# Performance work log

Hardware: AMD Instinct MI355X
Metric: run time of the kernel (lower is better)

Reference implementation:

```python
import jax, jax.numpy as jnp
import numpy as np

# ---- straight-through binary quantizers (custom VJP matches torch autograd.Functions) ----
@jax.custom_vjp
def bq(x):
    return jnp.sign(x)
def _bq_fwd(x):
    return jnp.sign(x), x
def _bq_bwd(x, g):
    return (g * ((x > -1.0) & (x < 1.0)).astype(g.dtype),)
bq.defvjp(_bq_fwd, _bq_bwd)

@jax.custom_vjp
def bq_quad(x):
    return jnp.sign(x)
def _bqq_fwd(x):
    return jnp.sign(x), x
def _bqq_bwd(x, g):
    return (jnp.maximum(2.0 - jnp.abs(2.0 * x), 0.0) * g,)
bq_quad.defvjp(_bqq_fwd, _bqq_bwd)

def bilinear(x, W, s, b):
    # BiLinear: row-centered sign weights scaled by learned per-row factor, sign activations
    Wc = W - jnp.mean(W, axis=-1, keepdims=True)
    Wb = s * bq(Wc)                      # (out, in)
    return bq(x) @ Wb.T + b

def selective_scan(u, delta, A, Bs, Cs, D, delta_bias):
    # u, delta: (B,K,Dn,L); A: (K,Dn,N); Bs,Cs: (B,K,N,L); D, delta_bias: (K,Dn)
    Bn, K, Dn, L = u.shape
    N = A.shape[-1]
    delta = jax.nn.softplus(delta + delta_bias[None, :, :, None])
    def step(h, inp):
        ut, dt, Bt, Ct = inp             # (B,K,Dn),(B,K,Dn),(B,K,N),(B,K,N)
        dA = jnp.exp(dt[..., None] * A[None])
        h = dA * h + (dt * ut)[..., None] * Bt[:, :, None, :]
        y = jnp.einsum('bkdn,bkn->bkd', h, Ct)
        return h, y
    h0 = jnp.zeros((Bn, K, Dn, N), u.dtype)
    _, ys = jax.lax.scan(step, h0,
                         (u.transpose(3, 0, 1, 2), delta.transpose(3, 0, 1, 2),
                          Bs.transpose(3, 0, 1, 2), Cs.transpose(3, 0, 1, 2)))
    y = ys.transpose(1, 2, 3, 0)         # (B,K,Dn,L)
    return y + D[None, :, :, None] * u

def _forward(x, W_in, b_in, s_in, move0_b, conv_W, conv_b, rp_b0, prelu_a, rp_b1,
             Wl, bl, sl, Wd, bd, sd, dt_bias, A_logs, Ds, ln_w, ln_b, W_out, b_out, s_out):
    Bn, H, Wi, dm = x.shape
    Dn = conv_W.shape[0]
    K = 4
    N = A_logs.shape[1]
    R = Wd.shape[2]
    L = H * Wi
    xz = bilinear(x, W_in, s_in, b_in)                  # (B,H,W,2*Dn)
    xp, z = jnp.split(xz, 2, axis=-1)
    xc = xp.transpose(0, 3, 1, 2)                       # (B,Dn,H,W)
    # BConv2d: move0 bias -> sign (quad STE) -> binary conv -> RPReLU -> residual
    t = bq_quad(xc + move0_b[None, :, None, None])
    sc = jax.lax.stop_gradient(jnp.mean(jnp.abs(conv_W), axis=(1, 2, 3), keepdims=True))
    cw = jnp.clip(conv_W, -1.0, 1.0)
    Wb = jax.lax.stop_gradient(sc * jnp.sign(conv_W) - cw) + cw
    t = jax.lax.conv_general_dilated(t, Wb, (1, 1), [(1, 1), (1, 1)],
                                     dimension_numbers=('NCHW', 'OIHW', 'NCHW'))
    t = t + conv_b[None, :, None, None]
    t = t + rp_b0[None, :, None, None]
    t = jnp.where(t >= 0, t, prelu_a[None, :, None, None] * t)
    t = t + rp_b1[None, :, None, None] + xc
    xconv = jax.nn.silu(t)
    # 4-direction scan inputs
    x_flat = xconv.reshape(Bn, Dn, L)
    x_tr = xconv.transpose(0, 1, 3, 2).reshape(Bn, Dn, L)
    x_hwwh = jnp.stack([x_flat, x_tr], axis=1)
    xs = jnp.concatenate([x_hwwh, jnp.flip(x_hwwh, axis=-1)], axis=1)   # (B,K,Dn,L)
    # NOTE: torch does .view(B,L,-1) on contiguous (B,Dn,L) slices = raw reshape (not transpose)
    xin = xs.reshape(Bn, K, L, Dn)
    x_dbl = jax.vmap(bilinear, in_axes=(1, 0, 0, 0), out_axes=1)(xin, Wl, sl, bl)  # (B,K,L,R+2N)
    x_dbl = x_dbl.transpose(0, 1, 3, 2)                                 # (B,K,R+2N,L)
    dts_r, Bs, Cs = jnp.split(x_dbl, [R, R + N], axis=2)
    dts_in = dts_r.reshape(Bn, K, L, R)  # raw reshape, matches torch .view
    dts = jax.vmap(bilinear, in_axes=(1, 0, 0, 0), out_axes=1)(dts_in, Wd, sd, bd)  # (B,K,L,Dn)
    dts = dts.transpose(0, 1, 3, 2)                                     # (B,K,Dn,L)
    A = -jnp.exp(A_logs).reshape(K, Dn, N)
    out_y = selective_scan(xs, dts, A, Bs, Cs, Ds.reshape(K, Dn), dt_bias.reshape(K, Dn))
    inv_y = jnp.flip(out_y[:, 2:4], axis=-1)
    wh_y = out_y[:, 1].reshape(Bn, Dn, Wi, H).transpose(0, 1, 3, 2).reshape(Bn, Dn, L)
    invwh_y = inv_y[:, 1].reshape(Bn, Dn, Wi, H).transpose(0, 1, 3, 2).reshape(Bn, Dn, L)
    y = out_y[:, 0] + inv_y[:, 0] + wh_y + invwh_y                      # (B,Dn,L)
    y = y.transpose(0, 2, 1).reshape(Bn, H, Wi, Dn)
    mu = jnp.mean(y, axis=-1, keepdims=True)
    var = jnp.var(y, axis=-1, keepdims=True)
    y = (y - mu) / jnp.sqrt(var + 1e-5) * ln_w + ln_b                   # LayerNorm eps=1e-5
    y = y * jax.nn.silu(z)
    return bilinear(y, W_out, s_out, b_out)

def setup_inputs():
    key = jax.random.key(0)
    ks = jax.random.split(key, 12)
    B, H, Wi, dm = 4, 64, 64, 96
    Dn, N, R, K = 192, 16, 6, 4
    u = lambda k, sh, a: jax.random.uniform(k, sh, jnp.float32, -a, a)
    x = jax.random.normal(ks[0], (B, H, Wi, dm), jnp.float32)
    W_in = u(ks[1], (2 * Dn, dm), 0.015)
    b_in = u(ks[2], (2 * Dn,), 0.01)
    s_in = jnp.mean(jnp.abs(W_in), axis=1, keepdims=True)
    move0_b = jnp.zeros((Dn,), jnp.float32)
    conv_W = 0.05 * jax.random.normal(ks[3], (Dn, Dn, 3, 3), jnp.float32)
    conv_b = u(ks[4], (Dn,), 0.01)
    rp_b0 = jnp.zeros((Dn,), jnp.float32)
    prelu_a = 0.25 * jnp.ones((Dn,), jnp.float32)
    rp_b1 = jnp.zeros((Dn,), jnp.float32)
    Wl = u(ks[5], (K, R + 2 * N, Dn), 0.015)
    bl = u(ks[6], (K, R + 2 * N), 0.01)
    sl = jnp.mean(jnp.abs(Wl), axis=2, keepdims=True)
    std = R ** -0.5
    Wd = u(ks[7], (K, Dn, R), std)
    bd = u(ks[8], (K, Dn), 0.01)
    sd = jnp.mean(jnp.abs(Wd), axis=2, keepdims=True)
    dt = jnp.exp(jax.random.uniform(ks[9], (K * Dn,), jnp.float32)
                 * (np.log(0.1) - np.log(0.001)) + np.log(0.001))
    dt = jnp.clip(dt, 1e-4, None)
    dt_bias = dt + jnp.log(-jnp.expm1(-dt))
    A_logs = jnp.tile(jnp.log(jnp.arange(1, N + 1, dtype=jnp.float32))[None, :], (K * Dn, 1))
    Ds = jnp.ones((K * Dn,), jnp.float32)
    ln_w = jnp.ones((Dn,), jnp.float32)
    ln_b = jnp.zeros((Dn,), jnp.float32)
    W_out = u(ks[10], (dm, Dn), 0.015)
    b_out = u(ks[11], (dm,), 0.01)
    s_out = jnp.mean(jnp.abs(W_out), axis=1, keepdims=True)
    return dict(x=x, W_in=W_in, b_in=b_in, s_in=s_in, move0_b=move0_b, conv_W=conv_W,
                conv_b=conv_b, rp_b0=rp_b0, prelu_a=prelu_a, rp_b1=rp_b1, Wl=Wl, bl=bl,
                sl=sl, Wd=Wd, bd=bd, sd=sd, dt_bias=dt_bias, A_logs=A_logs, Ds=Ds,
                ln_w=ln_w, ln_b=ln_b, W_out=W_out, b_out=b_out, s_out=s_out)

def reference(x, W_in, b_in, s_in, move0_b, conv_W, conv_b, rp_b0, prelu_a, rp_b1,
              Wl, bl, sl, Wd, bd, sd, dt_bias, A_logs, Ds, ln_w, ln_b, W_out, b_out, s_out):
    return _forward(x, W_in, b_in, s_in, move0_b, conv_W, conv_b, rp_b0, prelu_a, rp_b1,
                    Wl, bl, sl, Wd, bd, sd, dt_bias, A_logs, Ds, ln_w, ln_b, W_out, b_out, s_out)
```

## Files before the change

### kernel.cpp

```cpp
#include <hip/hip_runtime.h>
#include <math.h>
#include <stdint.h>

#define BB 4
#define HH 64
#define WW2 64
#define DM 96
#define DN 192
#define KK 4
#define NN 16
#define RR 6
#define LL 4096
#define RN 38

#define LOG2E 1.4426950408889634f
#define LN2   0.6931471805599453f

#define OFF_WDB      0
#define OFF_WCS      4608
#define OFF_WAUX     15360
#define OFF_WSC      16896
#define OFF_WBIB     17088
#define OFF_WOUTB    18240
#define OFF_WLBB     18816
#define OFF_XBP      19728
#define OFF_PXS      19728
#define OFF_PXIN     412944
#define OFF_XP       462096
#define OFF_XCONV    3607824
#define OFF_XCT      6753552
#define OFF_HEND     462096
#define OFF_YA       9899280
#define OFF_SSUM     22482192
#define OFF_GE       22875408
#define OFF_GSG      23268624

#define PLANE 4356
#define NCH 128
#define CHUNK 32

__device__ __forceinline__ float softplusf(float v) {
  return fmaxf(v, 0.f) + LN2 * log2f(1.f + exp2f(-fabsf(v) * LOG2E));
}
__device__ __forceinline__ float siluf(float v) {
  return v / (1.f + expf(-v));
}
__device__ __forceinline__ float waveAllSum(float s) {
  #pragma unroll
  for (int off = 32; off; off >>= 1) s += __shfl_xor(s, off, 64);
  return s;
}

__global__ __launch_bounds__(64) void k_prep(
    const float* __restrict__ W_in, const float* __restrict__ s_in,
    const float* __restrict__ W_out, const float* __restrict__ s_out,
    const float* __restrict__ Wl, const float* __restrict__ sl,
    const float* __restrict__ Wd, const float* __restrict__ sd,
    const float* __restrict__ convW, float* __restrict__ ws) {
  __shared__ float srow[1728];
  int r = blockIdx.x, lane = threadIdx.x;
  if (r < 384) {
    const float* row = W_in + r * DM;
    float s = 0.f;
    for (int c = lane; c < DM; c += 64) s += row[c];
    s = waveAllSum(s);
    float mean = s / (float)DM;
    if (lane < 3) {
      uint32_t wv = 0;
      #pragma unroll
      for (int i = 0; i < 32; ++i) wv |= (row[lane * 32 + i] - mean > 0.f ? 1u : 0u) << i;
      ((uint32_t*)(ws + OFF_WBIB))[r * 3 + lane] = wv;
    }
  } else if (r < 480) {
    int m = r - 384;
    const float* row = W_out + m * DN;
    float s = 0.f;
    for (int c = lane; c < DN; c += 64) s += row[c];
    s = waveAllSum(s);
    float mean = s / (float)DN;
    if (lane < 6) {
      uint32_t wv = 0;
      #pragma unroll
      for (int i = 0; i < 32; ++i) wv |= (row[lane * 32 + i] - mean > 0.f ? 1u : 0u) << i;
      ((uint32_t*)(ws + OFF_WOUTB))[m * 6 + lane] = wv;
    }
  } else if (r < 632) {
    int idx = r - 480;
    const float* row = Wl + idx * DN;
    float s = 0.f;
    for (int c = lane; c < DN; c += 64) s += row[c];
    s = waveAllSum(s);
    float mean = s / (float)DN;
    if (lane < 6) {
      uint32_t wv = 0;
      #pragma unroll
      for (int i = 0; i < 32; ++i) wv |= (row[lane * 32 + i] - mean > 0.f ? 1u : 0u) << i;
      ((uint32_t*)(ws + OFF_WLBB))[idx * 6 + lane] = wv;
    }
  } else if (r < 1400) {
    int idx = r - 632;
    const float* row = Wd + idx * RR;
    float s = (lane < RR) ? row[lane] : 0.f;
    s = waveAllSum(s);
    float mean = s / (float)RR;
    unsigned long long mb = __ballot((lane < RR) && (row[lane] - mean > 0.f));
    if (lane == 0) {
      ((uint32_t*)(ws + OFF_WDB))[idx] = (uint32_t)mb & 0x3Fu;
      (ws + OFF_WDB)[768 + idx] = sd[idx];
    }
  } else if (r < 1592) {
    int o = r - 1400;
    const float* row = convW + o * 1728;
    float s = 0.f;
    for (int j = lane; j < 1728; j += 64) {
      float v = row[j];
      srow[j] = v;
      s += fabsf(v);
    }
    s = waveAllSum(s);
    __syncthreads();
    float sc = s / 1728.f;
    uint32_t* wb = (uint32_t*)(ws + OFF_WCS);
    int* aux = (int*)(ws + OFF_WAUX);
    float* scf = ws + OFF_WSC;
    uint32_t word = 0;
    if (lane < 54) {
      int cw = lane / 9, tap = lane % 9;
      #pragma unroll
      for (int i = 0; i < 32; ++i)
        word |= (srow[(cw * 32 + i) * 9 + tap] > 0.f ? 1u : 0u) << i;
      wb[o * 56 + lane] = word;
    } else if (lane < 56) {
      wb[o * 56 + lane] = 0u;
    }
    int pc = (lane < 54) ? 2 * (int)__popc(word) - 32 : 0;
    int tapid = lane % 9;
    int wst = 0;
    #pragma unroll
    for (int cw = 0; cw < 6; ++cw) wst += __shfl(pc, cw * 9 + tapid, 64);
    int w_t[9];
    #pragma unroll
    for (int t9 = 0; t9 < 9; ++t9) w_t[t9] = __shfl(wst, t9, 64);
    if (lane == 0) {
      aux[o * 8 + 0] = w_t[0] + w_t[3] + w_t[6];
      aux[o * 8 + 1] = w_t[2] + w_t[5] + w_t[8];
      aux[o * 8 + 2] = w_t[0] + w_t[1] + w_t[2];
      aux[o * 8 + 3] = w_t[6] + w_t[7] + w_t[8];
      aux[o * 8 + 4] = w_t[0];
      aux[o * 8 + 5] = w_t[2];
      aux[o * 8 + 6] = w_t[6];
      aux[o * 8 + 7] = w_t[8];
      scf[o] = sc;
    }
  } else {
    int p = r - 1592;
    uint32_t* plane = (uint32_t*)(ws + OFF_XBP) + (size_t)p * PLANE;
    for (int i = lane; i < 66; i += 64) {
      plane[i] = 0u;
      plane[65 * 66 + i] = 0u;
    }
    for (int i = lane; i < 64; i += 64) {
      plane[(i + 1) * 66] = 0u;
      plane[(i + 1) * 66 + 65] = 0u;
    }
  }
}

__global__ __launch_bounds__(384) void k_bilin_in(
    const float* __restrict__ x, const float* __restrict__ b_in,
    const float* __restrict__ s_in, const float* __restrict__ move0,
    const float* __restrict__ ws, float* __restrict__ xp,
    uint32_t* __restrict__ pxin, uint32_t* __restrict__ xb) {
  __shared__ uint32_t spx[16 * 3];
  __shared__ float sxz[192 * 17];
  __shared__ float smv[DN];
  int p0 = blockIdx.x * 16;
  if (threadIdx.x < 48) {
    int pix = threadIdx.x / 3, wd = threadIdx.x % 3;
    const float* base = x + (size_t)(p0 + pix) * DM + wd * 32;
    uint32_t wv = 0;
    #pragma unroll
    for (int i = 0; i < 32; ++i) wv |= (base[i] > 0.f ? 1u : 0u) << i;
    spx[pix * 3 + wd] = wv;
  }
  if (threadIdx.x < DN) smv[threadIdx.x] = move0[threadIdx.x];
  __syncthreads();
  int half = threadIdx.x / 192;
  int o = threadIdx.x - half * 192;
  uint32_t w0, w1, w2;
  {
    const uint32_t* wb = (const uint32_t*)(ws + OFF_WBIB) + o * 3;
    w0 = wb[0]; w1 = wb[1]; w2 = wb[2];
  }
  float bias = b_in[o], sc = s_in[o];
  #pragma unroll
  for (int pp = 0; pp < 8; ++pp) {
    int pix = half * 8 + pp;
    int P = (int)__popc(spx[pix * 3 + 0] ^ w0) + (int)__popc(spx[pix * 3 + 1] ^ w1) +
            (int)__popc(spx[pix * 3 + 2] ^ w2);
    sxz[o * 17 + pix] = bias + sc * (float)(DM - 2 * P);
  }
  __syncthreads();
  int b = p0 >> 12, l0 = p0 & 4095;
  for (int f = threadIdx.x; f < DN * 16; f += 384) {
    int od = f >> 4, pix = f & 15;
    xp[((size_t)(b * DN + od)) * LL + l0 + pix] = sxz[od * 17 + pix];
  }
  if (threadIdx.x < 48) {
    int pix = threadIdx.x / 3, wd = threadIdx.x % 3;
    pxin[(size_t)(p0 + pix) * 3 + wd] = spx[pix * 3 + wd];
  }
  if (threadIdx.x < 96) {
    int pix = threadIdx.x / 6, cw = threadIdx.x % 6;
    uint32_t wv = 0;
    #pragma unroll
    for (int i = 0; i < 32; ++i) {
      int dch = cw * 32 + i;
      wv |= ((sxz[dch * 17 + pix] + smv[dch] > 0.f) ? 1u : 0u) << i;
    }
    int l = l0 + pix, h = l >> 6, w = l & 63;
    uint32_t* plane = xb + (size_t)(b * 6 + cw) * PLANE;
    plane[(h + 1) * 66 + 1 + w] = wv;
  }
}

__global__ __launch_bounds__(256) void k_conv(
    const uint32_t* __restrict__ xb, const float* __restrict__ xc,
    const uint32_t* __restrict__ wbits, const int* __restrict__ aux,
    const float* __restrict__ scf, const float* __restrict__ conv_b,
    const float* __restrict__ rp_b0, const float* __restrict__ prelu_a,
    const float* __restrict__ rp_b1, float* __restrict__ xconv) {
  int ocg = blockIdx.x & 3;
  int og = (blockIdx.x >> 2) & 3;
  int stripe = (blockIdx.x >> 4) & 15;
  int b = blockIdx.x >> 8;
  int w = threadIdx.x & 63, r = threadIdx.x >> 6;
  int h = stripe * 4 + r;
  int obase = og * 48 + ocg * 12;

  __shared__ uint32_t swb[12 * 56];
  __shared__ int saux[12 * 8];
  __shared__ float sconst[12 * 4];
  for (int i = threadIdx.x; i < 12 * 56; i += 256) swb[i] = wbits[obase * 56 + i];
  for (int i = threadIdx.x; i < 12 * 8; i += 256) saux[i] = aux[obase * 8 + i];
  if (threadIdx.x < 12) {
    int o = obase + threadIdx.x;
    sconst[threadIdx.x * 4 + 0] = scf[o];
    sconst[threadIdx.x * 4 + 1] = conv_b[o] + rp_b0[o];
    sconst[threadIdx.x * 4 + 2] = prelu_a[o];
    sconst[threadIdx.x * 4 + 3] = rp_b1[o];
  }

  uint32_t xw[6][9];
  const uint32_t* xpb = xb + (size_t)b * 6 * PLANE;
  #pragma unroll
  for (int cw = 0; cw < 6; ++cw) {
    const uint32_t* plane = xpb + cw * PLANE + (h + 1) * 66 + (w + 1);
    #pragma unroll
    for (int dy = 0; dy < 3; ++dy) {
      #pragma unroll
      for (int dx = 0; dx < 3; ++dx)
        xw[cw][dy * 3 + dx] = plane[(dy - 1) * 66 + (dx - 1)];
    }
  }
  bool isL = (w == 0), isR = (w == 63);
  bool isT = (h == 0), isB = (h == 63);
  const float* xcp = xc + ((size_t)(b * DN + obase)) * LL + h * 64 + w;
  float* xop = xconv + ((size_t)(b * DN + obase)) * LL + h * 64 + w;
  __syncthreads();

  #pragma unroll 1
  for (int oc = 0; oc < 12; ++oc) {
    const uint32_t* wp = &swb[oc * 56];
    int P = 0;
    #pragma unroll
    for (int cw = 0; cw < 6; ++cw) {
      int pp = 0;
      #pragma unroll
      for (int t = 0; t < 9; ++t) pp += (int)__popc(wp[cw * 9 + t] ^ xw[cw][t]);
      P += pp;
    }
    int corr = isL ? saux[oc * 8 + 0] : (isR ? saux[oc * 8 + 1] : 0);
    if (isT) {
      corr += saux[oc * 8 + 2];
      if (isL) corr -= saux[oc * 8 + 4];
      if (isR) corr -= saux[oc * 8 + 5];
    }
    if (isB) {
      corr += saux[oc * 8 + 3];
      if (isL) corr -= saux[oc * 8 + 6];
      if (isR) corr -= saux[oc * 8 + 7];
    }
    float acc = sconst[oc * 4 + 0] * (float)(1728 - 2 * P + corr);
    float t = acc + sconst[oc * 4 + 1];
    t = (t >= 0.f) ? t : sconst[oc * 4 + 2] * t;
    t += sconst[oc * 4 + 3] + *xcp;
    *xop = siluf(t);
    xcp += LL; xop += LL;
  }
}

__global__ __launch_bounds__(256) void k_bits_xpose(const float* __restrict__ xconv,
                                                    uint32_t* __restrict__ pxs,
                                                    float* __restrict__ xct) {
  __shared__ float tile[64][65];
  if (blockIdx.x < 768) {
    int bd = blockIdx.x;
    int b = bd / DN, dch = bd - b * DN;
    const float* img = xconv + (size_t)bd * LL;
    for (int i = threadIdx.x; i < LL; i += 256)
      tile[i >> 6][i & 63] = img[i];
    __syncthreads();
    int lane = threadIdx.x & 63;
    #pragma unroll
    for (int k = 0; k < 4; ++k) {
      size_t wbase = ((size_t)((b * KK + k) * DN + dch)) * 128;
      for (int j = threadIdx.x; j < LL; j += 256) {
        float v;
        if (k == 0)      v = tile[j >> 6][j & 63];
        else if (k == 1) v = tile[j & 63][j >> 6];
        else if (k == 2) { int t2 = 4095 - j; v = tile[t2 >> 6][t2 & 63]; }
        else             { int t2 = 4095 - j; v = tile[t2 & 63][t2 >> 6]; }
        unsigned long long m = __ballot(v > 0.f);
        if (lane == 0)       pxs[wbase + (j >> 5)] = (uint32_t)m;
        else if (lane == 32) pxs[wbase + (j >> 5)] = (uint32_t)(m >> 32);
      }
    }
  } else {
    int idx = blockIdx.x - 768;
    int ts = idx & 63;
    int rest = idx >> 6;
    int dg = rest % 3;
    int b = rest / 3;
    int d0 = dg * 64, t0 = ts * 64;
    for (int i = threadIdx.x; i < 4096; i += 256) {
      int dd = i >> 6, tt = i & 63;
      tile[dd][tt] = xconv[((size_t)(b * DN + d0 + dd)) * LL + t0 + tt];
    }
    __syncthreads();
    for (int i = threadIdx.x; i < 4096; i += 256) {
      int tt = i >> 6, dd = i & 63;
      xct[((size_t)(b * LL + t0 + tt)) * DN + d0 + dd] = tile[dd][tt];
    }
  }
}

__device__ __forceinline__ void rpowers(float r, float* a) {
  float r2 = r * r, r3 = r2 * r, r4 = r2 * r2, r8 = r4 * r4;
  a[0] = r;       a[1] = r2;      a[2] = r3;      a[3] = r4;
  a[4] = r4 * r;  a[5] = r4 * r2; a[6] = r4 * r3; a[7] = r8;
  a[8] = r8 * r;  a[9] = r8 * r2; a[10] = r8 * r3; a[11] = r8 * r4;
  a[12] = r8 * a[4]; a[13] = r8 * a[5]; a[14] = r8 * a[6]; a[15] = r8 * r8;
}

__device__ __forceinline__ int rowstep(int k) {
  return (k == 0) ? DN : (k == 1) ? 64 * DN : (k == 2) ? -DN : -64 * DN;
}
__device__ __forceinline__ int rowbase(int k, int tb) {
  int r0 = (k >= 2) ? (4095 - tb) : tb;
  if (k & 1) r0 = ((r0 & 63) << 6) | (r0 >> 6);
  return r0 * DN;
}

__global__ __launch_bounds__(192) void k_scan_a(
    const float* __restrict__ xct, const uint32_t* __restrict__ pxs,
    const float* __restrict__ ws, const float* __restrict__ bl,
    const float* __restrict__ sl, const float* __restrict__ bd,
    const float* __restrict__ dt_bias, const float* __restrict__ A_logs,
    float* __restrict__ hend, float* __restrict__ Ssum) {
  int c = blockIdx.x & (NCH - 1);
  int bk = blockIdx.x >> 7;
  int k = bk & 3, b = bk >> 2;
  int d = threadIdx.x;
  int t0 = c << 5;
  __shared__ uint32_t sdtm[CHUNK];
  __shared__ uint32_t spxr[CHUNK * 6];
  __shared__ uint32_t swl[RN * 6];
  __shared__ float sblv[RN], sslv[RN];
  __shared__ float4 sB4[CHUNK * 4];
  __shared__ float sDV[7 * 192], sR[7 * 192];
  float* sBf = (float*)sB4;
  const uint32_t* ppx = pxs + (size_t)bk * 24576;
  spxr[d] = ppx[t0 * 6 + d];
  for (int i = d; i < RN * 6; i += 192) swl[i] = ((const uint32_t*)(ws + OFF_WLBB))[k * RN * 6 + i];
  if (d < RN) {
    sblv[d] = bl[k * RN + d];
    sslv[d] = sl[k * RN + d];
  }
  __syncthreads();
  if (d < CHUNK) {
    uint32_t m = 0;
    int fbase = (t0 + d) * 6;
    #pragma unroll
    for (int r = 0; r < 6; ++r) {
      int f = fbase + r;
      int o = f >> 12, l = f & 4095;
      const uint32_t* prow = ppx + l * 6;
      int P = 0;
      #pragma unroll
      for (int j = 0; j < 6; ++j) P += (int)__popc(prow[j] ^ swl[o * 6 + j]);
      float val = sblv[o] + sslv[o] * (float)(DN - 2 * P);
      m |= (val > 0.f ? 1u : 0u) << r;
    }
    sdtm[d] = m;
  }
  for (int i = d; i < CHUNK * 16; i += 192) {
    int t = i >> 4, n = i & 15;
    int o = RR + n;
    int P = 0;
    #pragma unroll
    for (int j = 0; j < 6; ++j) P += (int)__popc(spxr[t * 6 + j] ^ swl[o * 6 + j]);
    sBf[t * 16 + n] = sblv[o] + sslv[o] * (float)(DN - 2 * P);
  }
  uint32_t w6 = ((const uint32_t*)(ws + OFF_WDB))[k * DN + d];
  float sdvv = (ws + OFF_WDB)[768 + k * DN + d];
  float biasd = bd[k * DN + d] + dt_bias[k * DN + d];
  #pragma unroll
  for (int pc = 0; pc < 7; ++pc) {
    float dv = softplusf(biasd + sdvv * (float)(RR - 2 * pc));
    sDV[pc * 192 + d] = dv;
    sR[pc * 192 + d] = exp2f(-dv * LOG2E);
  }
  float Araw[16];
  bool fok = true;
  {
    const float* ap = A_logs + (k * DN + d) * NN;
    #pragma unroll
    for (int n = 0; n < NN; ++n) {
      Araw[n] = -expf(ap[n]);
      fok = fok && (fabsf(Araw[n] + (float)(n + 1)) < 1e-3f);
    }
  }
  bool fastpath = (__ballot(fok) == ~0ull);
  float An[16];
  if (!fastpath) {
    #pragma unroll
    for (int n = 0; n < NN; ++n) An[n] = Araw[n] * LOG2E;
  }
  float h[16];
  #pragma unroll
  for (int n = 0; n < NN; ++n) h[n] = 0.f;
  float S = 0.f;
  int ubase = b * (LL * DN) + d;
  int rstep = rowstep(k);
  __syncthreads();
  #pragma unroll 1
  for (int seg = 0; seg < 4; ++seg) {
    int rbase = rowbase(k, t0 + seg * 8);
    float uu[8];
    #pragma unroll
    for (int i = 0; i < 8; ++i) uu[i] = xct[ubase + rbase + i * rstep];
    #pragma unroll
    for (int i = 0; i < 8; ++i) {
      int t = seg * 8 + i;
      float uv = uu[i];
      int pc = (int)__popc(sdtm[t] ^ w6);
      float dv = sDV[pc * 192 + d];
      S += dv;
      float du = dv * uv;
      if (fastpath) {
        float rv = sR[pc * 192 + d];
        float a[16];
        rpowers(rv, a);
        #pragma unroll
        for (int g = 0; g < 4; ++g) {
          float4 bv = sB4[t * 4 + g];
          h[4 * g + 0] = a[4 * g + 0] * h[4 * g + 0] + du * bv.x;
          h[4 * g + 1] = a[4 * g + 1] * h[4 * g + 1] + du * bv.y;
          h[4 * g + 2] = a[4 * g + 2] * h[4 * g + 2] + du * bv.z;
          h[4 * g + 3] = a[4 * g + 3] * h[4 * g + 3] + du * bv.w;
        }
      } else {
        #pragma unroll
        for (int g = 0; g < 4; ++g) {
          float4 bv = sB4[t * 4 + g];
          float a0 = exp2f(dv * An[4 * g + 0]);
          float a1 = exp2f(dv * An[4 * g + 1]);
          float a2 = exp2f(dv * An[4 * g + 2]);
          float a3 = exp2f(dv * An[4 * g + 3]);
          h[4 * g + 0] = a0 * h[4 * g + 0] + du * bv.x;
          h[4 * g + 1] = a1 * h[4 * g + 1] + du * bv.y;
          h[4 * g + 2] = a2 * h[4 * g + 2] + du * bv.z;
          h[4 * g + 3] = a3 * h[4 * g + 3] + du * bv.w;
        }
      }
    }
  }
  float* hp = hend + (size_t)c * 49152 + (size_t)(bk * DN + d) * 16;
  #pragma unroll
  for (int n = 0; n < NN; n += 4)
    *(float4*)(hp + n) = make_float4(h[n], h[n + 1], h[n + 2], h[n + 3]);
  Ssum[c * 3072 + bk * DN + d] = S;
}

__global__ __launch_bounds__(256) void k_scan_b1(
    const float* __restrict__ A_logs, const float* __restrict__ Ssum,
    float* __restrict__ hend, float* __restrict__ gE, float* __restrict__ gSG) {
  int g = blockIdx.x / 192;
  int blk = blockIdx.x - g * 192;
  int tid = blk * 256 + threadIdx.x;
  int bkd = tid >> 4, n = tid & 15;
  int bk = bkd / DN, d = bkd - bk * DN;
  int k = bk & 3;
  float An2 = -expf(A_logs[(k * DN + d) * NN + n]) * LOG2E;
  int c0 = g * 16;
  float E = 0.f, SG = 0.f;
  float Sc = Ssum[c0 * 3072 + bkd];
  float he = hend[(size_t)c0 * 49152 + tid];
  #pragma unroll 1
  for (int j = 0; j < 16; ++j) {
    int c = c0 + j;
    float Sn = 0.f, hn = 0.f;
    if (j < 15) {
      Sn = Ssum[(c + 1) * 3072 + bkd];
      hn = hend[(size_t)(c + 1) * 49152 + tid];
    }
    hend[(size_t)c * 49152 + tid] = E;
    E = exp2f(An2 * Sc) * E + he;
    SG += Sc;
    Sc = Sn; he = hn;
  }
  gE[(size_t)g * 49152 + tid] = E;
  if (n == 0) gSG[g * 3072 + bkd] = SG;
}

__global__ __launch_bounds__(256) void k_scan_b2(
    const float* __restrict__ A_logs, const float* __restrict__ Ssum,
    float* __restrict__ hend, const float* __restrict__ gE,
    const float* __restrict__ gSG) {
  int g = blockIdx.x / 192;
  if (g == 0) return;
  int blk = blockIdx.x - g * 192;
  int tid = blk * 256 + threadIdx.x;
  int bkd = tid >> 4, n = tid & 15;
  int bk = bkd / DN, d = bkd - bk * DN;
  int k = bk & 3;
  float An2 = -expf(A_logs[(k * DN + d) * NN + n]) * LOG2E;
  float H = 0.f;
  #pragma unroll 1
  for (int j = 0; j < g; ++j) {
    float Aj = exp2f(An2 * gSG[j * 3072 + bkd]);
    H = Aj * H + gE[(size_t)j * 49152 + tid];
  }
  int c0 = g * 16;
  float Spre = 0.f;
  #pragma unroll 1
  for (int j = 0; j < 16; ++j) {
    int c = c0 + j;
    hend[(size_t)c * 49152 + tid] += exp2f(An2 * Spre) * H;
    Spre += Ssum[c * 3072 + bkd];
  }
}

__global__ __launch_bounds__(192) void k_scan_c(
    const float* __restrict__ xct, const uint32_t* __restrict__ pxs,
    const float* __restrict__ ws, const float* __restrict__ bl,
    const float* __restrict__ sl, const float* __restrict__ bd,
    const float* __restrict__ dt_bias, const float* __restrict__ A_logs,
    const float* __restrict__ Ds, float* __restrict__ yA,
    const float* __restrict__ h0buf) {
  int c = blockIdx.x & (NCH - 1);
  int bk = blockIdx.x >> 7;
  int k = bk & 3, b = bk >> 2;
  int d = threadIdx.x;
  int t0 = c << 5;
  __shared__ uint32_t sdtm[CHUNK];
  __shared__ uint32_t spxr[CHUNK * 6];
  __shared__ uint32_t swl[RN * 6];
  __shared__ float sblv[RN], sslv[RN];
  __shared__ float4 sB4[CHUNK * 4];
  __shared__ float4 sC4[CHUNK * 4];
  __shared__ float sDV[7 * 192], sR[7 * 192];
  float* sBf = (float*)sB4;
  float* sCf = (float*)sC4;
  const uint32_t* ppx = pxs + (size_t)bk * 24576;
  spxr[d] = ppx[t0 * 6 + d];
  for (int i = d; i < RN * 6; i += 192) swl[i] = ((const uint32_t*)(ws + OFF_WLBB))[k * RN * 6 + i];
  if (d < RN) {
    sblv[d] = bl[k * RN + d];
    sslv[d] = sl[k * RN + d];
  }
  __syncthreads();
  if (d < CHUNK) {
    uint32_t m = 0;
    int fbase = (t0 + d) * 6;
    #pragma unroll
    for (int r = 0; r < 6; ++r) {
      int f = fbase + r;
      int o = f >> 12, l = f & 4095;
      const uint32_t* prow = ppx + l * 6;
      int P = 0;
      #pragma unroll
      for (int j = 0; j < 6; ++j) P += (int)__popc(prow[j] ^ swl[o * 6 + j]);
      float val = sblv[o] + sslv[o] * (float)(DN - 2 * P);
      m |= (val > 0.f ? 1u : 0u) << r;
    }
    sdtm[d] = m;
  }
  for (int i = d; i < CHUNK * 32; i += 192) {
    int t = i >> 5, nn = i & 31;
    int o = RR + nn;
    int P = 0;
    #pragma unroll
    for (int j = 0; j < 6; ++j) P += (int)__popc(spxr[t * 6 + j] ^ swl[o * 6 + j]);
    float val = sblv[o] + sslv[o] * (float)(DN - 2 * P);
    if (nn < 16) sBf[t * 16 + nn] = val;
    else         sCf[t * 16 + (nn - 16)] = val;
  }
  uint32_t w6 = ((const uint32_t*)(ws + OFF_WDB))[k * DN + d];
  float sdvv = (ws + OFF_WDB)[768 + k * DN + d];
  float biasd = bd[k * DN + d] + dt_bias[k * DN + d];
  float Dd = Ds[k * DN + d];
  #pragma unroll
  for (int pc = 0; pc < 7; ++pc) {
    float dv = softplusf(biasd + sdvv * (float)(RR - 2 * pc));
    sDV[pc * 192 + d] = dv;
    sR[pc * 192 + d] = exp2f(-dv * LOG2E);
  }
  float Araw[16];
  bool fok = true;
  {
    const float* ap = A_logs + (k * DN + d) * NN;
    #pragma unroll
    for (int n = 0; n < NN; ++n) {
      Araw[n] = -expf(ap[n]);
      fok = fok && (fabsf(Araw[n] + (float)(n + 1)) < 1e-3f);
    }
  }
  bool fastpath = (__ballot(fok) == ~0ull);
  float An[16];
  if (!fastpath) {
    #pragma unroll
    for (int n = 0; n < NN; ++n) An[n] = Araw[n] * LOG2E;
  }
  float h[16];
  {
    const float* hp = h0buf + (size_t)c * 49152 + (size_t)(bk * DN + d) * 16;
    #pragma unroll
    for (int n = 0; n < NN; n += 4) {
      float4 v = *(const float4*)(hp + n);
      h[n] = v.x; h[n + 1] = v.y; h[n + 2] = v.z; h[n + 3] = v.w;
    }
  }
  int ubase = b * (LL * DN) + d;
  int ybase = bk * (LL * DN) + d;
  int rstep = rowstep(k);
  __syncthreads();
  #pragma unroll 1
  for (int seg = 0; seg < 4; ++seg) {
    int rbase = rowbase(k, t0 + seg * 8);
    float uu[8];
    #pragma unroll
    for (int i = 0; i < 8; ++i) uu[i] = xct[ubase + rbase + i * rstep];
    #pragma unroll
    for (int i = 0; i < 8; ++i) {
      int t = seg * 8 + i;
      float uv = uu[i];
      int pc = (int)__popc(sdtm[t] ^ w6);
      float dv = sDV[pc * 192 + d];
      float du = dv * uv;
      float p[4];
      #pragma unroll
      for (int g = 0; g < 4; ++g) p[g] = 0.f;
      if (fastpath) {
        float rv = sR[pc * 192 + d];
        float a[16];
        rpowers(rv, a);
        #pragma unroll
        for (int g = 0; g < 4; ++g) {
          float4 bv = sB4[t * 4 + g];
          float4 cv = sC4[t * 4 + g];
          h[4 * g + 0] = a[4 * g + 0] * h[4 * g + 0] + du * bv.x;
          h[4 * g + 1] = a[4 * g + 1] * h[4 * g + 1] + du * bv.y;
          h[4 * g + 2] = a[4 * g + 2] * h[4 * g + 2] + du * bv.z;
          h[4 * g + 3] = a[4 * g + 3] * h[4 * g + 3] + du * bv.w;
          p[g] += cv.x * h[4 * g + 0];
          p[g] += cv.y * h[4 * g + 1];
          p[g] += cv.z * h[4 * g + 2];
          p[g] += cv.w * h[4 * g + 3];
        }
      } else {
        #pragma unroll
        for (int g = 0; g < 4; ++g) {
          float4 bv = sB4[t * 4 + g];
          float4 cv = sC4[t * 4 + g];
          float a0 = exp2f(dv * An[4 * g + 0]);
          float a1 = exp2f(dv * An[4 * g + 1]);
          float a2 = exp2f(dv * An[4 * g + 2]);
          float a3 = exp2f(dv * An[4 * g + 3]);
          h[4 * g + 0] = a0 * h[4 * g + 0] + du * bv.x;
          h[4 * g + 1] = a1 * h[4 * g + 1] + du * bv.y;
          h[4 * g + 2] = a2 * h[4 * g + 2] + du * bv.z;
          h[4 * g + 3] = a3 * h[4 * g + 3] + du * bv.w;
          p[g] += cv.x * h[4 * g + 0];
          p[g] += cv.y * h[4 * g + 1];
          p[g] += cv.z * h[4 * g + 2];
          p[g] += cv.w * h[4 * g + 3];
        }
      }
      float yv = Dd * uv + ((p[0] + p[1]) + (p[2] + p[3]));
      yA[ybase + rbase + i * rstep] = yv;
    }
  }
}

__global__ __launch_bounds__(256) void k_ln_out(
    const float* __restrict__ yA, const uint32_t* __restrict__ pxin,
    const float* __restrict__ b_in, const float* __restrict__ s_in,
    const float* __restrict__ ln_w, const float* __restrict__ ln_b,
    const float* __restrict__ ws, const float* __restrict__ b_out,
    const float* __restrict__ s_out, float* __restrict__ out) {
  __shared__ float ty[16 * 193];
  __shared__ float ps[256];
  __shared__ float smu[16], srs[16];
  __shared__ float slw[DN], slb[DN];
  __shared__ uint32_t ybits[16 * 6];
  __shared__ uint32_t swo[96 * 6];
  __shared__ float sb[96], ssc[96];
  __shared__ uint32_t szw[DN * 3];
  __shared__ float szb[DN], szs[DN];
  __shared__ uint32_t spxt[16 * 3];
  int b = blockIdx.x >> 8;
  int l0 = (blockIdx.x & 255) << 4;
  if (threadIdx.x < DN) {
    slw[threadIdx.x] = ln_w[threadIdx.x];
    slb[threadIdx.x] = ln_b[threadIdx.x];
    szb[threadIdx.x] = b_in[DN + threadIdx.x];
    szs[threadIdx.x] = s_in[DN + threadIdx.x];
  }
  for (int i = threadIdx.x; i < 96 * 6; i += 256) swo[i] = ((const uint32_t*)(ws + OFF_WOUTB))[i];
  for (int i = threadIdx.x; i < DN * 3; i += 256) szw[i] = ((const uint32_t*)(ws + OFF_WBIB))[DN * 3 + i];
  if (threadIdx.x < 96) {
    sb[threadIdx.x] = b_out[threadIdx.x];
    ssc[threadIdx.x] = s_out[threadIdx.x];
  }
  if (threadIdx.x < 48) spxt[threadIdx.x] = pxin[(size_t)(b * LL + l0) * 3 + threadIdx.x];
  const float* y0 = yA + (size_t)(b * 4 + 0) * (LL * DN) + (size_t)l0 * DN;
  const float* y1 = yA + (size_t)(b * 4 + 1) * (LL * DN) + (size_t)l0 * DN;
  const float* y2 = yA + (size_t)(b * 4 + 2) * (LL * DN) + (size_t)l0 * DN;
  const float* y3 = yA + (size_t)(b * 4 + 3) * (LL * DN) + (size_t)l0 * DN;
  for (int i = threadIdx.x; i < 16 * DN; i += 256) {
    int lc = i / DN, dd = i - lc * DN;
    size_t off = (size_t)lc * DN + dd;
    ty[lc * 193 + dd] = y0[off] + y1[off] + y2[off] + y3[off];
  }
  __syncthreads();
  int lc = threadIdx.x & 15, part = threadIdx.x >> 4;
  float s = 0.f;
  for (int d = part * 12; d < part * 12 + 12; ++d) s += ty[lc * 193 + d];
  ps[threadIdx.x] = s;
  __syncthreads();
  if (threadIdx.x < 16) {
    float m = 0.f;
    #pragma unroll
    for (int p = 0; p < 16; ++p) m += ps[p * 16 + threadIdx.x];
    smu[threadIdx.x] = m / (float)DN;
  }
  __syncthreads();
  float mu = smu[lc];
  float q = 0.f;
  for (int d = part * 12; d < part * 12 + 12; ++d) {
    float v = ty[lc * 193 + d] - mu; q += v * v;
  }
  ps[threadIdx.x] = q;
  __syncthreads();
  if (threadIdx.x < 16) {
    float vv = 0.f;
    #pragma unroll
    for (int p = 0; p < 16; ++p) vv += ps[p * 16 + threadIdx.x];
    srs[threadIdx.x] = rsqrtf(vv / (float)DN + 1e-5f);
  }
  __syncthreads();
  if (threadIdx.x < 16 * 6) {
    int lc2 = threadIdx.x / 6, wd = threadIdx.x % 6;
    float mu2 = smu[lc2], rs2 = srs[lc2];
    uint32_t px0 = spxt[lc2 * 3 + 0], px1 = spxt[lc2 * 3 + 1], px2 = spxt[lc2 * 3 + 2];
    uint32_t wv = 0;
    #pragma unroll
    for (int i = 0; i < 32; ++i) {
      int dd = wd * 32 + i;
      float lnv = (ty[lc2 * 193 + dd] - mu2) * rs2 * slw[dd] + slb[dd];
      int P = (int)__popc(px0 ^ szw[dd * 3 + 0]) + (int)__popc(px1 ^ szw[dd * 3 + 1]) +
              (int)__popc(px2 ^ szw[dd * 3 + 2]);
      float zv = szb[dd] + szs[dd] * (float)(DM - 2 * P);
      wv |= ((lnv * zv > 0.f) ? 1u : 0u) << i;
    }
    ybits[lc2 * 6 + wd] = wv;
  }
  __syncthreads();
  float* op = out + (size_t)(b * LL + l0) * DM;
  for (int oi = threadIdx.x; oi < 16 * DM; oi += 256) {
    int pr = oi / DM, m = oi % DM;
    int P = 0;
    #pragma unroll
    for (int j = 0; j < 6; ++j) P += (int)__popc(ybits[pr * 6 + j] ^ swo[m * 6 + j]);
    op[(size_t)pr * DM + m] = sb[m] + ssc[m] * (float)(DN - 2 * P);
  }
}

extern "C" void kernel_launch(void* const* d_in, const int* in_sizes, int n_in,
                              void* d_out, int out_size, void* d_ws, size_t ws_size,
                              hipStream_t stream) {
  const float* x       = (const float*)d_in[0];
  const float* W_in    = (const float*)d_in[1];
  const float* b_in    = (const float*)d_in[2];
  const float* s_in    = (const float*)d_in[3];
  const float* move0_b = (const float*)d_in[4];
  const float* conv_W  = (const float*)d_in[5];
  const float* conv_b  = (const float*)d_in[6];
  const float* rp_b0   = (const float*)d_in[7];
  const float* prelu_a = (const float*)d_in[8];
  const float* rp_b1   = (const float*)d_in[9];
  const float* Wl      = (const float*)d_in[10];
  const float* bl      = (const float*)d_in[11];
  const float* sl      = (const float*)d_in[12];
  const float* Wd      = (const float*)d_in[13];
  const float* bd      = (const float*)d_in[14];
  const float* sd      = (const float*)d_in[15];
  const float* dt_bias = (const float*)d_in[16];
  const float* A_logs  = (const float*)d_in[17];
  const float* Ds      = (const float*)d_in[18];
  const float* ln_w    = (const float*)d_in[19];
  const float* ln_b    = (const float*)d_in[20];
  const float* W_out   = (const float*)d_in[21];
  const float* b_out   = (const float*)d_in[22];
  const float* s_out   = (const float*)d_in[23];
  float* ws  = (float*)d_ws;
  float* out = (float*)d_out;

  hipLaunchKernelGGL(k_prep, dim3(1616), dim3(64), 0, stream,
                     W_in, s_in, W_out, s_out, Wl, sl, Wd, sd, conv_W, ws);
  hipLaunchKernelGGL(k_bilin_in, dim3(1024), dim3(384), 0, stream,
                     x, b_in, s_in, move0_b, ws, ws + OFF_XP,
                     (uint32_t*)(ws + OFF_PXIN), (uint32_t*)(ws + OFF_XBP));
  hipLaunchKernelGGL(k_conv, dim3(1024), dim3(256), 0, stream,
                     (const uint32_t*)(ws + OFF_XBP), ws + OFF_XP,
                     (const uint32_t*)(ws + OFF_WCS), (const int*)(ws + OFF_WAUX),
                     ws + OFF_WSC, conv_b, rp_b0, prelu_a, rp_b1,
                     ws + OFF_XCONV);
  hipLaunchKernelGGL(k_bits_xpose, dim3(1536), dim3(256), 0, stream,
                     ws + OFF_XCONV, (uint32_t*)(ws + OFF_PXS), ws + OFF_XCT);
  hipLaunchKernelGGL(k_scan_a, dim3(2048), dim3(192), 0, stream,
                     ws + OFF_XCT, (const uint32_t*)(ws + OFF_PXS), ws, bl, sl,
                     bd, dt_bias, A_logs, ws + OFF_HEND, ws + OFF_SSUM);
  hipLaunchKernelGGL(k_scan_b1, dim3(1536), dim3(256), 0, stream,
                     A_logs, ws + OFF_SSUM, ws + OFF_HEND, ws + OFF_GE, ws + OFF_GSG);
  hipLaunchKernelGGL(k_scan_b2, dim3(1536), dim3(256), 0, stream,
                     A_logs, ws + OFF_SSUM, ws + OFF_HEND, ws + OFF_GE, ws + OFF_GSG);
  hipLaunchKernelGGL(k_scan_c, dim3(2048), dim3(192), 0, stream,
                     ws + OFF_XCT, (const uint32_t*)(ws + OFF_PXS), ws, bl, sl,
                     bd, dt_bias, A_logs, Ds, ws + OFF_YA, ws + OFF_HEND);
  hipLaunchKernelGGL(k_ln_out, dim3(1024), dim3(256), 0, stream,
                     ws + OFF_YA, (const uint32_t*)(ws + OFF_PXIN), b_in, s_in,
                     ln_w, ln_b, ws, b_out, s_out, out);
}
```

Baseline: 277.3 us.

## Recompute input projection inside conv and use fewer, longer scan chunks

The float input-projection tensor is no longer written by the bilinear kernel and read back by the conv kernel. Instead the conv kernel recomputes each channel's value from the packed sign bits and binarized weights with a popcount. Separately, the chunked selective scan now uses 64 chunks of 64 steps instead of 128 chunks of 32. This halves the chunk-state buffers and the work in the cross-chunk combine passes, but each scan block runs a longer serial loop and fewer blocks are launched.

```diff
diff --git a/kernel.cpp b/kernel.cpp
--- a/kernel.cpp
+++ b/kernel.cpp
@@ -26,18 +26,18 @@
 #define OFF_XBP      19728
 #define OFF_PXS      19728
 #define OFF_PXIN     412944
-#define OFF_XP       462096
+#define OFF_HEND     462096
 #define OFF_XCONV    3607824
 #define OFF_XCT      6753552
-#define OFF_HEND     462096
 #define OFF_YA       9899280
 #define OFF_SSUM     22482192
-#define OFF_GE       22875408
-#define OFF_GSG      23268624
+#define OFF_GE       22678800
+#define OFF_GSG      23072016
 
 #define PLANE 4356
-#define NCH 128
-#define CHUNK 32
+#define NCH 64
+#define CHUNK 64
+#define NSEG 8
 
 __device__ __forceinline__ float softplusf(float v) {
   return fmaxf(v, 0.f) + LN2 * log2f(1.f + exp2f(-fabsf(v) * LOG2E));
@@ -169,7 +169,7 @@
 __global__ __launch_bounds__(384) void k_bilin_in(
     const float* __restrict__ x, const float* __restrict__ b_in,
     const float* __restrict__ s_in, const float* __restrict__ move0,
-    const float* __restrict__ ws, float* __restrict__ xp,
+    const float* __restrict__ ws,
     uint32_t* __restrict__ pxin, uint32_t* __restrict__ xb) {
   __shared__ uint32_t spx[16 * 3];
   __shared__ float sxz[192 * 17];
@@ -202,10 +202,6 @@
   }
   __syncthreads();
   int b = p0 >> 12, l0 = p0 & 4095;
-  for (int f = threadIdx.x; f < DN * 16; f += 384) {
-    int od = f >> 4, pix = f & 15;
-    xp[((size_t)(b * DN + od)) * LL + l0 + pix] = sxz[od * 17 + pix];
-  }
   if (threadIdx.x < 48) {
     int pix = threadIdx.x / 3, wd = threadIdx.x % 3;
     pxin[(size_t)(p0 + pix) * 3 + wd] = spx[pix * 3 + wd];
@@ -225,11 +221,13 @@
 }
 
 __global__ __launch_bounds__(256) void k_conv(
-    const uint32_t* __restrict__ xb, const float* __restrict__ xc,
+    const uint32_t* __restrict__ xb, const uint32_t* __restrict__ pxin,
+    const uint32_t* __restrict__ wbib,
     const uint32_t* __restrict__ wbits, const int* __restrict__ aux,
     const float* __restrict__ scf, const float* __restrict__ conv_b,
     const float* __restrict__ rp_b0, const float* __restrict__ prelu_a,
-    const float* __restrict__ rp_b1, float* __restrict__ xconv) {
+    const float* __restrict__ rp_b1, const float* __restrict__ b_in,
+    const float* __restrict__ s_in, float* __restrict__ xconv) {
   int ocg = blockIdx.x & 3;
   int og = (blockIdx.x >> 2) & 3;
   int stripe = (blockIdx.x >> 4) & 15;
@@ -241,14 +239,19 @@
   __shared__ uint32_t swb[12 * 56];
   __shared__ int saux[12 * 8];
   __shared__ float sconst[12 * 4];
+  __shared__ uint32_t swib[12 * 3];
+  __shared__ float sbv[12], ssv[12];
   for (int i = threadIdx.x; i < 12 * 56; i += 256) swb[i] = wbits[obase * 56 + i];
   for (int i = threadIdx.x; i < 12 * 8; i += 256) saux[i] = aux[obase * 8 + i];
+  if (threadIdx.x < 36) swib[threadIdx.x] = wbib[obase * 3 + threadIdx.x];
   if (threadIdx.x < 12) {
     int o = obase + threadIdx.x;
     sconst[threadIdx.x * 4 + 0] = scf[o];
     sconst[threadIdx.x * 4 + 1] = conv_b[o] + rp_b0[o];
     sconst[threadIdx.x * 4 + 2] = prelu_a[o];
     sconst[threadIdx.x * 4 + 3] = rp_b1[o];
+    sbv[threadIdx.x] = b_in[o];
+    ssv[threadIdx.x] = s_in[o];
   }
 
   uint32_t xw[6][9];
@@ -263,10 +266,15 @@
         xw[cw][dy * 3 + dx] = plane[(dy - 1) * 66 + (dx - 1)];
     }
   }
+  int l = h * 64 + w;
+  uint32_t px0, px1, px2;
+  {
+    const uint32_t* pxp = pxin + ((size_t)(b * LL + l)) * 3;
+    px0 = pxp[0]; px1 = pxp[1]; px2 = pxp[2];
+  }
   bool isL = (w == 0), isR = (w == 63);
   bool isT = (h == 0), isB = (h == 63);
-  const float* xcp = xc + ((size_t)(b * DN + obase)) * LL + h * 64 + w;
-  float* xop = xconv + ((size_t)(b * DN + obase)) * LL + h * 64 + w;
+  float* xop = xconv + ((size_t)(b * DN + obase)) * LL + l;
   __syncthreads();
 
   #pragma unroll 1
@@ -291,12 +299,15 @@
       if (isL) corr -= saux[oc * 8 + 6];
       if (isR) corr -= saux[oc * 8 + 7];
     }
+    int Pr = (int)__popc(px0 ^ swib[oc * 3 + 0]) + (int)__popc(px1 ^ swib[oc * 3 + 1]) +
+             (int)__popc(px2 ^ swib[oc * 3 + 2]);
+    float xcv = sbv[oc] + ssv[oc] * (float)(DM - 2 * Pr);
     float acc = sconst[oc * 4 + 0] * (float)(1728 - 2 * P + corr);
     float t = acc + sconst[oc * 4 + 1];
     t = (t >= 0.f) ? t : sconst[oc * 4 + 2] * t;
-    t += sconst[oc * 4 + 3] + *xcp;
+    t += sconst[oc * 4 + 3] + xcv;
     *xop = siluf(t);
-    xcp += LL; xop += LL;
+    xop += LL;
   }
 }
 
@@ -369,10 +380,10 @@
     const float* __restrict__ dt_bias, const float* __restrict__ A_logs,
     float* __restrict__ hend, float* __restrict__ Ssum) {
   int c = blockIdx.x & (NCH - 1);
-  int bk = blockIdx.x >> 7;
+  int bk = blockIdx.x >> 6;
   int k = bk & 3, b = bk >> 2;
   int d = threadIdx.x;
-  int t0 = c << 5;
+  int t0 = c << 6;
   __shared__ uint32_t sdtm[CHUNK];
   __shared__ uint32_t spxr[CHUNK * 6];
   __shared__ uint32_t swl[RN * 6];
@@ -381,7 +392,7 @@
   __shared__ float sDV[7 * 192], sR[7 * 192];
   float* sBf = (float*)sB4;
   const uint32_t* ppx = pxs + (size_t)bk * 24576;
-  spxr[d] = ppx[t0 * 6 + d];
+  for (int i = d; i < CHUNK * 6; i += 192) spxr[i] = ppx[t0 * 6 + i];
   for (int i = d; i < RN * 6; i += 192) swl[i] = ((const uint32_t*)(ws + OFF_WLBB))[k * RN * 6 + i];
   if (d < RN) {
     sblv[d] = bl[k * RN + d];
@@ -445,7 +456,7 @@
   int rstep = rowstep(k);
   __syncthreads();
   #pragma unroll 1
-  for (int seg = 0; seg < 4; ++seg) {
+  for (int seg = 0; seg < NSEG; ++seg) {
     int rbase = rowbase(k, t0 + seg * 8);
     float uu[8];
     #pragma unroll
@@ -503,15 +514,15 @@
   int bk = bkd / DN, d = bkd - bk * DN;
   int k = bk & 3;
   float An2 = -expf(A_logs[(k * DN + d) * NN + n]) * LOG2E;
-  int c0 = g * 16;
+  int c0 = g * 8;
   float E = 0.f, SG = 0.f;
   float Sc = Ssum[c0 * 3072 + bkd];
   float he = hend[(size_t)c0 * 49152 + tid];
   #pragma unroll 1
-  for (int j = 0; j < 16; ++j) {
+  for (int j = 0; j < 8; ++j) {
     int c = c0 + j;
     float Sn = 0.f, hn = 0.f;
-    if (j < 15) {
+    if (j < 7) {
       Sn = Ssum[(c + 1) * 3072 + bkd];
       hn = hend[(size_t)(c + 1) * 49152 + tid];
     }
@@ -542,10 +553,10 @@
     float Aj = exp2f(An2 * gSG[j * 3072 + bkd]);
     H = Aj * H + gE[(size_t)j * 49152 + tid];
   }
-  int c0 = g * 16;
+  int c0 = g * 8;
   float Spre = 0.f;
   #pragma unroll 1
-  for (int j = 0; j < 16; ++j) {
+  for (int j = 0; j < 8; ++j) {
     int c = c0 + j;
     hend[(size_t)c * 49152 + tid] += exp2f(An2 * Spre) * H;
     Spre += Ssum[c * 3072 + bkd];
@@ -560,10 +571,10 @@
     const float* __restrict__ Ds, float* __restrict__ yA,
     const float* __restrict__ h0buf) {
   int c = blockIdx.x & (NCH - 1);
-  int bk = blockIdx.x >> 7;
+  int bk = blockIdx.x >> 6;
   int k = bk & 3, b = bk >> 2;
   int d = threadIdx.x;
-  int t0 = c << 5;
+  int t0 = c << 6;
   __shared__ uint32_t sdtm[CHUNK];
   __shared__ uint32_t spxr[CHUNK * 6];
   __shared__ uint32_t swl[RN * 6];
@@ -574,7 +585,7 @@
   float* sBf = (float*)sB4;
   float* sCf = (float*)sC4;
   const uint32_t* ppx = pxs + (size_t)bk * 24576;
-  spxr[d] = ppx[t0 * 6 + d];
+  for (int i = d; i < CHUNK * 6; i += 192) spxr[i] = ppx[t0 * 6 + i];
   for (int i = d; i < RN * 6; i += 192) swl[i] = ((const uint32_t*)(ws + OFF_WLBB))[k * RN * 6 + i];
   if (d < RN) {
     sblv[d] = bl[k * RN + d];
@@ -647,7 +658,7 @@
   int rstep = rowstep(k);
   __syncthreads();
   #pragma unroll 1
-  for (int seg = 0; seg < 4; ++seg) {
+  for (int seg = 0; seg < NSEG; ++seg) {
     int rbase = rowbase(k, t0 + seg * 8);
     float uu[8];
     #pragma unroll
@@ -831,23 +842,25 @@
   hipLaunchKernelGGL(k_prep, dim3(1616), dim3(64), 0, stream,
                      W_in, s_in, W_out, s_out, Wl, sl, Wd, sd, conv_W, ws);
   hipLaunchKernelGGL(k_bilin_in, dim3(1024), dim3(384), 0, stream,
-                     x, b_in, s_in, move0_b, ws, ws + OFF_XP,
+                     x, b_in, s_in, move0_b, ws,
                      (uint32_t*)(ws + OFF_PXIN), (uint32_t*)(ws + OFF_XBP));
   hipLaunchKernelGGL(k_conv, dim3(1024), dim3(256), 0, stream,
-                     (const uint32_t*)(ws + OFF_XBP), ws + OFF_XP,
+                     (const uint32_t*)(ws + OFF_XBP),
+                     (const uint32_t*)(ws + OFF_PXIN),
+                     (const uint32_t*)(ws + OFF_WBIB),
                      (const uint32_t*)(ws + OFF_WCS), (const int*)(ws + OFF_WAUX),
                      ws + OFF_WSC, conv_b, rp_b0, prelu_a, rp_b1,
-                     ws + OFF_XCONV);
+                     b_in, s_in, ws + OFF_XCONV);
   hipLaunchKernelGGL(k_bits_xpose, dim3(1536), dim3(256), 0, stream,
                      ws + OFF_XCONV, (uint32_t*)(ws + OFF_PXS), ws + OFF_XCT);
-  hipLaunchKernelGGL(k_scan_a, dim3(2048), dim3(192), 0, stream,
+  hipLaunchKernelGGL(k_scan_a, dim3(1024), dim3(192), 0, stream,
                      ws + OFF_XCT, (const uint32_t*)(ws + OFF_PXS), ws, bl, sl,
                      bd, dt_bias, A_logs, ws + OFF_HEND, ws + OFF_SSUM);
   hipLaunchKernelGGL(k_scan_b1, dim3(1536), dim3(256), 0, stream,
                      A_logs, ws + OFF_SSUM, ws + OFF_HEND, ws + OFF_GE, ws + OFF_GSG);
   hipLaunchKernelGGL(k_scan_b2, dim3(1536), dim3(256), 0, stream,
                      A_logs, ws + OFF_SSUM, ws + OFF_HEND, ws + OFF_GE, ws + OFF_GSG);
-  hipLaunchKernelGGL(k_scan_c, dim3(2048), dim3(192), 0, stream,
+  hipLaunchKernelGGL(k_scan_c, dim3(1024), dim3(192), 0, stream,
                      ws + OFF_XCT, (const uint32_t*)(ws + OFF_PXS), ws, bl, sl,
                      bd, dt_bias, A_logs, Ds, ws + OFF_YA, ws + OFF_HEND);
   hipLaunchKernelGGL(k_ln_out, dim3(1024), dim3(256), 0, stream,
```

Measured after the change: 278.7 us. No clear change (+0.5%).
